# Kernel tuning notes

Measured on AMD Instinct MI355X. Metric: run time of the kernel, lower is better.

Reference implementation:

```python
import jax, jax.numpy as jnp
import numpy as np

B, T, C, H, N = 4, 1024, 2048, 32, 64
DFF, DW, DV, DA, DG = 8192, 64, 32, 64, 128
GN_EPS = 64e-5  # RWKV7 ln_x GroupNorm eps


def _ln(x, w, b, eps=1e-5):
    m = x.mean(-1, keepdims=True)
    v = ((x - m) ** 2).mean(-1, keepdims=True)
    return (x - m) / jnp.sqrt(v + eps) * w + b


def _block(x, v_first, att_shift, ffn_shift, wkv_state,
           ln1_w, ln1_b, ln2_w, ln2_b,
           x_r, x_w, x_k, x_v, x_a, x_g,
           Wr, Wk, Wv, Wo,
           w0, w1, w2, v0, v1, v2, a0, a1, a2, g1, g2,
           k_k, k_a, r_k, lnx_w, lnx_b,
           ffn_xk, Wk_ffn, Wv_ffn):
    # ----- TimeMix -----
    xn = _ln(x, ln1_w, ln1_b)
    xx = jnp.concatenate([att_shift[:, None, :], xn[:, :-1]], axis=1) - xn
    xr = xn + xx * x_r
    xw = xn + xx * x_w
    xk_ = xn + xx * x_k
    xv = xn + xx * x_v
    xa = xn + xx * x_a
    xg = xn + xx * x_g

    r = xr @ Wr
    w = -jax.nn.softplus(-(w0 + jnp.tanh(xw @ w1) @ w2)) - 0.5  # <= -0.5
    k = xk_ @ Wk
    v = xv @ Wv
    # layer_id != 0: interpolate toward v_first
    v = v + (v_first - v) * jax.nn.sigmoid(v0 + (xv @ v1) @ v2)
    a = jax.nn.sigmoid(a0 + (xa @ a1) @ a2)
    g = jax.nn.sigmoid(xg @ g1) @ g2

    kk = (k * k_k).reshape(B, T, H, N)
    kk = kk / jnp.maximum(jnp.linalg.norm(kk, axis=-1, keepdims=True), 1e-12)
    k = k * (1.0 + (a - 1.0) * k_a)

    rh = r.reshape(B, T, H, N)
    wh = jnp.exp(-jnp.exp(w.reshape(B, T, H, N)))  # decay in (0,1)
    kh = k.reshape(B, T, H, N)
    vh = v.reshape(B, T, H, N)
    ah = a.reshape(B, T, H, N)
    aa = -kk
    bb = kk * ah

    def step(S, inp):
        # S: [B,H,N(value),N(key)]
        r_t, w_t, k_t, v_t, a_t, b_t = inp
        sa = jnp.einsum('bhvk,bhk->bhv', S, a_t)
        S = S * w_t[:, :, None, :] + sa[..., None] * b_t[:, :, None, :] + v_t[..., None] * k_t[:, :, None, :]
        y = jnp.einsum('bhvk,bhk->bhv', S, r_t)
        return S, y

    tm = lambda z: jnp.swapaxes(z, 0, 1)  # [B,T,H,N] -> [T,B,H,N]
    S_new, ys = jax.lax.scan(step, wkv_state, (tm(rh), tm(wh), tm(kh), tm(vh), tm(aa), tm(bb)))
    x_wkv = jnp.swapaxes(ys, 0, 1).reshape(B, T, C)

    # GroupNorm over H groups of size N (RWKV7 ln_x)
    xh = x_wkv.reshape(B, T, H, N)
    mu = xh.mean(-1, keepdims=True)
    var = ((xh - mu) ** 2).mean(-1, keepdims=True)
    x_wkv = ((xh - mu) / jnp.sqrt(var + GN_EPS)).reshape(B, T, C) * lnx_w + lnx_b

    resid = ((rh * kh * r_k).sum(-1, keepdims=True) * vh).reshape(B, T, C)
    x_wkv = x_wkv + resid
    att_out = (x_wkv * g) @ Wo
    x1 = x + att_out

    # ----- ChannelMix -----
    xn2 = _ln(x1, ln2_w, ln2_b)
    xx2 = jnp.concatenate([ffn_shift[:, None, :], xn2[:, :-1]], axis=1) - xn2
    xkf = xn2 + xx2 * ffn_xk
    kf = jnp.square(jax.nn.relu(xkf @ Wk_ffn))
    x_out = x1 + kf @ Wv_ffn
    return x_out, S_new


def setup_inputs() -> dict:
    ks = jax.random.split(jax.random.key(0), 48)
    rn = lambda i, sh, s=1.0: jax.random.normal(ks[i], sh, dtype=jnp.float32) * s
    return {
        'x': rn(0, (B, T, C)), 'v_first': rn(1, (B, T, C)),
        'att_shift': rn(2, (B, C)), 'ffn_shift': rn(3, (B, C)),
        'wkv_state': jnp.zeros((B, H, N, N), jnp.float32),
        'ln1_w': jnp.ones((C,), jnp.float32), 'ln1_b': jnp.zeros((C,), jnp.float32),
        'ln2_w': jnp.ones((C,), jnp.float32), 'ln2_b': jnp.zeros((C,), jnp.float32),
        'x_r': rn(4, (C,), 0.3), 'x_w': rn(5, (C,), 0.3), 'x_k': rn(6, (C,), 0.3),
        'x_v': rn(7, (C,), 0.3), 'x_a': rn(8, (C,), 0.3), 'x_g': rn(9, (C,), 0.3),
        'Wr': rn(10, (C, C), 0.02), 'Wk': rn(11, (C, C), 0.02),
        'Wv': rn(12, (C, C), 0.02), 'Wo': rn(13, (C, C), 0.02),
        'w0': rn(14, (C,), 0.3), 'w1': rn(15, (C, DW), 0.02), 'w2': rn(16, (DW, C), 0.02),
        'v0': rn(17, (C,), 0.3), 'v1': rn(18, (C, DV), 0.02), 'v2': rn(19, (DV, C), 0.02),
        'a0': rn(20, (C,), 0.3), 'a1': rn(21, (C, DA), 0.02), 'a2': rn(22, (DA, C), 0.02),
        'g1': rn(23, (C, DG), 0.02), 'g2': rn(24, (DG, C), 0.02),
        'k_k': rn(25, (C,), 0.1) + 0.7, 'k_a': rn(26, (C,), 0.1) + 0.7, 'r_k': rn(27, (H, N), 0.1),
        'lnx_w': jnp.ones((C,), jnp.float32), 'lnx_b': jnp.zeros((C,), jnp.float32),
        'ffn_xk': rn(28, (C,), 0.3), 'Wk_ffn': rn(29, (C, DFF), 0.02), 'Wv_ffn': rn(30, (DFF, C), 0.02),
    }


def reference(x, v_first, att_shift, ffn_shift, wkv_state,
              ln1_w, ln1_b, ln2_w, ln2_b,
              x_r, x_w, x_k, x_v, x_a, x_g,
              Wr, Wk, Wv, Wo,
              w0, w1, w2, v0, v1, v2, a0, a1, a2, g1, g2,
              k_k, k_a, r_k, lnx_w, lnx_b,
              ffn_xk, Wk_ffn, Wv_ffn):
    return _block(x, v_first, att_shift, ffn_shift, wkv_state,
                  ln1_w, ln1_b, ln2_w, ln2_b,
                  x_r, x_w, x_k, x_v, x_a, x_g,
                  Wr, Wk, Wv, Wo,
                  w0, w1, w2, v0, v1, v2, a0, a1, a2, g1, g2,
                  k_k, k_a, r_k, lnx_w, lnx_b,
                  ffn_xk, Wk_ffn, Wv_ffn)
```

## Files before the change

kernel.cpp:

```cpp
#include <hip/hip_runtime.h>
#include <cstdint>


typedef __attribute__((ext_vector_type(4))) float f32x4;
typedef __attribute__((ext_vector_type(8))) __bf16 bf16x8;
typedef __attribute__((ext_vector_type(8))) unsigned short us8;

#define DEV __device__ __forceinline__

DEV unsigned short f2b(float f) {
  union { float f; unsigned u; } v; v.f = f;
  unsigned r = v.u + 0x7fffu + ((v.u >> 16) & 1u);
  return (unsigned short)(r >> 16);
}
DEV float b2f(unsigned short u) {
  union { unsigned u; float f; } v; v.u = (unsigned)u << 16;
  return v.f;
}

DEV void gload16(const void* g, void* l) {
  void* gg = const_cast<void*>(g);
  __builtin_amdgcn_global_load_lds(
      (__attribute__((address_space(1))) unsigned int*)gg,
      (__attribute__((address_space(3))) unsigned int*)l, 16, 0, 0);
}

DEV float red8(float v) {
  v += __shfl_xor(v, 1);
  v += __shfl_xor(v, 2);
  v += __shfl_xor(v, 4);
  return v;
}


__global__ void k_transpose4(const float* __restrict__ s0,
                             const float* __restrict__ s1,
                             const float* __restrict__ s2,
                             const float* __restrict__ s3,
                             unsigned short* __restrict__ d0,
                             unsigned short* __restrict__ d1,
                             unsigned short* __restrict__ d2,
                             unsigned short* __restrict__ d3) {
  __shared__ float tile[32][33];
  const int z = blockIdx.z;
  const float* src = z == 0 ? s0 : z == 1 ? s1 : z == 2 ? s2 : s3;
  unsigned short* dst = z == 0 ? d0 : z == 1 ? d1 : z == 2 ? d2 : d3;
  const int c0 = blockIdx.x * 32, r0 = blockIdx.y * 32;
  const int tx = threadIdx.x, ty = threadIdx.y;
  for (int i = ty; i < 32; i += 8)
    tile[i][tx] = src[(size_t)(r0 + i) * 2048 + c0 + tx];
  __syncthreads();
  for (int i = ty; i < 32; i += 8)
    dst[(size_t)(c0 + i) * 2048 + r0 + tx] = f2b(tile[tx][i]);
}

__global__ void k_transpose(const float* __restrict__ src,
                            unsigned short* __restrict__ dst, int R, int Cc) {
  __shared__ float tile[32][33];
  const int c0 = blockIdx.x * 32, r0 = blockIdx.y * 32;
  const int tx = threadIdx.x, ty = threadIdx.y;
  for (int i = ty; i < 32; i += 8)
    tile[i][tx] = src[(size_t)(r0 + i) * Cc + c0 + tx];
  __syncthreads();
  for (int i = ty; i < 32; i += 8)
    dst[(size_t)(c0 + i) * R + r0 + tx] = f2b(tile[tx][i]);
}

__global__ void k_prep(const float* __restrict__ w1, const float* __restrict__ a1,
                       const float* __restrict__ v1, const float* __restrict__ g1,
                       const float* __restrict__ xw, const float* __restrict__ xa,
                       const float* __restrict__ xv, const float* __restrict__ xg,
                       const float* __restrict__ w2, const float* __restrict__ a2,
                       const float* __restrict__ v2, const float* __restrict__ g2,
                       unsigned short* __restrict__ dcat,
                       unsigned short* __restrict__ dup) {
  int i = blockIdx.x * 256 + threadIdx.x;
  if (i < 384 * 4096) {
    const int j = i >> 12, c = i & 4095;
    float val = 0.f;
    if (j < 288) {
      const float* W; const float* mix; int jj, D;
      if (j < 64)       { W = w1; mix = xw; jj = j;       D = 64;  }
      else if (j < 128) { W = a1; mix = xa; jj = j - 64;  D = 64;  }
      else if (j < 160) { W = v1; mix = xv; jj = j - 128; D = 32;  }
      else              { W = g1; mix = xg; jj = j - 160; D = 128; }
      const int cc = c & 2047;
      val = W[(size_t)cc * D + jj];
      if (c >= 2048) val *= mix[cc];
    }
    dcat[i] = f2b(val);
    return;
  }
  i -= 384 * 4096;
  if (i >= 8192 * 288) return;
  const int n = i / 288, k = i - n * 288;
  const int p = n >> 11, j = n & 2047;
  float val = 0.f;
  if (p == 0)      { if (k < 64)              val = w2[(size_t)k * 2048 + j]; }
  else if (p == 1) { if (k >= 64 && k < 128)  val = a2[(size_t)(k - 64) * 2048 + j]; }
  else if (p == 2) { if (k >= 128 && k < 160) val = v2[(size_t)(k - 128) * 2048 + j]; }
  else             { if (k >= 160)            val = g2[(size_t)(k - 160) * 2048 + j]; }
  dup[i] = f2b(val);
}


DEV void breduce2(float& a, float& b, float* rbuf) {
#pragma unroll
  for (int m = 1; m < 64; m <<= 1) { a += __shfl_xor(a, m); b += __shfl_xor(b, m); }
  const int wid = threadIdx.x >> 6, lane = threadIdx.x & 63;
  if (lane == 0) { rbuf[wid] = a; rbuf[4 + wid] = b; }
  __syncthreads();
  a = rbuf[0] + rbuf[1] + rbuf[2] + rbuf[3];
  b = rbuf[4] + rbuf[5] + rbuf[6] + rbuf[7];
  __syncthreads();
}

__global__ __launch_bounds__(256)
void k_ln1_mix(const float* __restrict__ x, const float* __restrict__ shift,
               const float* __restrict__ lw, const float* __restrict__ lb,
               const float* __restrict__ mr, const float* __restrict__ mk,
               const float* __restrict__ mv,
               unsigned short* __restrict__ A2, unsigned short* __restrict__ xrb,
               unsigned short* __restrict__ xkb, unsigned short* __restrict__ xvb) {
  __shared__ float rbuf[8];
  const int m = blockIdx.x, tid = threadIdx.x;
  const int b = m >> 10, t = m & 1023;
  const float* xt = x + (size_t)m * 2048 + tid * 8;
  const float* xp = (t > 0) ? (x + (size_t)(m - 1) * 2048 + tid * 8)
                            : (shift + (size_t)b * 2048 + tid * 8);
  float vt[8], vp[8];
  *(float4*)&vt[0] = *(const float4*)(xt);
  *(float4*)&vt[4] = *(const float4*)(xt + 4);
  *(float4*)&vp[0] = *(const float4*)(xp);
  *(float4*)&vp[4] = *(const float4*)(xp + 4);
  float st = 0.f, sp = 0.f;
#pragma unroll
  for (int i = 0; i < 8; ++i) { st += vt[i]; sp += vp[i]; }
  breduce2(st, sp, rbuf);
  const float mt_ = st * (1.f / 2048.f), mp_ = sp * (1.f / 2048.f);
  float qt = 0.f, qp = 0.f;
#pragma unroll
  for (int i = 0; i < 8; ++i) {
    float d0 = vt[i] - mt_; qt += d0 * d0;
    float d1 = vp[i] - mp_; qp += d1 * d1;
  }
  breduce2(qt, qp, rbuf);
  const float rt = rsqrtf(qt * (1.f / 2048.f) + 1e-5f);
  const float rp = rsqrtf(qp * (1.f / 2048.f) + 1e-5f);
  const bool lnp = (t > 0);
#pragma unroll
  for (int i = 0; i < 8; ++i) {
    const int c = tid * 8 + i;
    const float wv = lw[c], bv = lb[c];
    const float xn = (vt[i] - mt_) * rt * wv + bv;
    const float pn = lnp ? ((vp[i] - mp_) * rp * wv + bv) : vp[i];
    const float xx = pn - xn;
    A2[(size_t)m * 4096 + c] = f2b(xn);
    A2[(size_t)m * 4096 + 2048 + c] = f2b(xx);
    xrb[(size_t)m * 2048 + c] = f2b(xn + xx * mr[c]);
    xkb[(size_t)m * 2048 + c] = f2b(xn + xx * mk[c]);
    xvb[(size_t)m * 2048 + c] = f2b(xn + xx * mv[c]);
  }
}

__global__ __launch_bounds__(256)
void k_ln2_mix(const float* __restrict__ x1, const float* __restrict__ shift,
               const float* __restrict__ lw, const float* __restrict__ lb,
               const float* __restrict__ mk, unsigned short* __restrict__ xkf) {
  __shared__ float rbuf[8];
  const int m = blockIdx.x, tid = threadIdx.x;
  const int b = m >> 10, t = m & 1023;
  const float* xt = x1 + (size_t)m * 2048 + tid * 8;
  const float* xp = (t > 0) ? (x1 + (size_t)(m - 1) * 2048 + tid * 8)
                            : (shift + (size_t)b * 2048 + tid * 8);
  float vt[8], vp[8];
  *(float4*)&vt[0] = *(const float4*)(xt);
  *(float4*)&vt[4] = *(const float4*)(xt + 4);
  *(float4*)&vp[0] = *(const float4*)(xp);
  *(float4*)&vp[4] = *(const float4*)(xp + 4);
  float st = 0.f, sp = 0.f;
#pragma unroll
  for (int i = 0; i < 8; ++i) { st += vt[i]; sp += vp[i]; }
  breduce2(st, sp, rbuf);
  const float mt_ = st * (1.f / 2048.f), mp_ = sp * (1.f / 2048.f);
  float qt = 0.f, qp = 0.f;
#pragma unroll
  for (int i = 0; i < 8; ++i) {
    float d0 = vt[i] - mt_; qt += d0 * d0;
    float d1 = vp[i] - mp_; qp += d1 * d1;
  }
  breduce2(qt, qp, rbuf);
  const float rt = rsqrtf(qt * (1.f / 2048.f) + 1e-5f);
  const float rp = rsqrtf(qp * (1.f / 2048.f) + 1e-5f);
  const bool lnp = (t > 0);
#pragma unroll
  for (int i = 0; i < 8; ++i) {
    const int c = tid * 8 + i;
    const float wv = lw[c], bv = lb[c];
    const float xn = (vt[i] - mt_) * rt * wv + bv;
    const float pn = lnp ? ((vp[i] - mp_) * rp * wv + bv) : vp[i];
    xkf[(size_t)m * 2048 + c] = f2b(xn + (pn - xn) * mk[c]);
  }
}


constexpr int EP_F32 = 0, EP_B16 = 1, EP_RELU2 = 5, EP_ADDF = 6, EP_HACT = 7;

template <int EP>
DEV void ep_store(float acc, long row, long c, long ldc, float* Co,
                  unsigned short* Cob, const float* bias, const float* e0f,
                  const unsigned short* e0b) {
  const long idx = row * ldc + c;
  (void)bias; (void)e0b;
  if constexpr (EP == EP_F32) {
    Co[idx] = acc;
  } else if constexpr (EP == EP_B16) {
    Cob[idx] = f2b(acc);
  } else if constexpr (EP == EP_RELU2) {
    const float r = fmaxf(acc, 0.f);
    Cob[idx] = f2b(r * r);
  } else if constexpr (EP == EP_ADDF) {
    Co[idx] = acc + e0f[idx];
  } else if constexpr (EP == EP_HACT) {
    float vv = acc;
    if (c < 64) vv = tanhf(vv);
    else if (c >= 160) vv = 1.f / (1.f + expf(-vv));
    Cob[idx] = f2b(vv);
  }
}


template <int EP>
__global__ __launch_bounds__(256)
void gemm_bt(const unsigned short* __restrict__ A, long lda,
             const unsigned short* __restrict__ Bt, long ldb, long N, long K,
             long ldc, float* __restrict__ Co, unsigned short* __restrict__ Cob,
             const float* __restrict__ bias, const float* __restrict__ e0f,
             const unsigned short* __restrict__ e0b) {
  __shared__ unsigned short As[4096];
  __shared__ unsigned short Bs[4096];
  const int tid = threadIdx.x;
  const int wid = tid >> 6, lane = tid & 63;
  const long row0 = (long)blockIdx.x * 128, col0 = (long)blockIdx.y * 128;
  const int wm = (wid >> 1) * 64, wn = (wid & 1) * 64;
  f32x4 acc[4][4] = {};
  const int sr = tid >> 2, sk = (tid & 3) * 8;
  const unsigned short* gA = A + (row0 + sr) * lda + sk;
  const unsigned short* gB = Bt + (col0 + sr) * ldb + sk;
  unsigned short* lA = As + wid * 512;
  unsigned short* lB = Bs + wid * 512;
  const int fr = lane & 15, fk = (lane >> 4) * 8;

  for (long kb = 0; kb < K; kb += 32) {
    gload16(gA + kb, lA);
    gload16(gA + kb + 64 * lda, lA + 2048);
    gload16(gB + kb, lB);
    gload16(gB + kb + 64 * ldb, lB + 2048);
    __syncthreads();
    bf16x8 af[4], bq[4];
#pragma unroll
    for (int mt = 0; mt < 4; ++mt)
      af[mt] = *(const bf16x8*)(As + (wm + mt * 16 + fr) * 32 + fk);
#pragma unroll
    for (int nt = 0; nt < 4; ++nt)
      bq[nt] = *(const bf16x8*)(Bs + (wn + nt * 16 + fr) * 32 + fk);
#pragma unroll
    for (int mt = 0; mt < 4; ++mt)
#pragma unroll
      for (int nt = 0; nt < 4; ++nt)
        acc[mt][nt] = __builtin_amdgcn_mfma_f32_16x16x32_bf16(
            af[mt], bq[nt], acc[mt][nt], 0, 0, 0);
    __syncthreads();
  }
  const int fq = lane >> 4;
#pragma unroll
  for (int mt = 0; mt < 4; ++mt) {
#pragma unroll
    for (int nt = 0; nt < 4; ++nt) {
      const long c = col0 + wn + nt * 16 + fr;
      if (c < N) {
        const long rb = row0 + wm + mt * 16 + fq * 4;
#pragma unroll
        for (int rg = 0; rg < 4; ++rg)
          ep_store<EP>(acc[mt][nt][rg], rb + rg, c, ldc, Co, Cob, bias, e0f, e0b);
      }
    }
  }
}


template <int EP>
__global__ __launch_bounds__(256)
void gemm3(const unsigned short* __restrict__ A, long lda,
           const unsigned short* __restrict__ Bt, long ldb, long K, long ldc,
           float* __restrict__ Co, unsigned short* __restrict__ Cob,
           const float* __restrict__ e0f) {
  __shared__ unsigned short As[2][4096];
  __shared__ unsigned short Bs[2][4096];
  const int tid = threadIdx.x;
  const int wid = tid >> 6, lane = tid & 63;
  const long row0 = (long)blockIdx.x * 128, col0 = (long)blockIdx.y * 128;
  const int wm = (wid >> 1) * 64, wn = (wid & 1) * 64;
  f32x4 acc[4][4] = {};
  const int srow = tid >> 2;
  const int scol = 8 * ((tid & 3) ^ (srow & 3));
  const unsigned short* gA = A + (row0 + srow) * lda + scol;
  const unsigned short* gB = Bt + (col0 + srow) * ldb + scol;
  const int fr = lane & 15, fc = lane >> 4;

#define STAGE3(buf, kb)                                         \
  {                                                             \
    gload16(gA + (kb), &As[buf][0] + wid * 512);                \
    gload16(gA + (kb) + 64 * lda, &As[buf][2048] + wid * 512);  \
    gload16(gB + (kb), &Bs[buf][0] + wid * 512);                \
    gload16(gB + (kb) + 64 * ldb, &Bs[buf][2048] + wid * 512);  \
  }

  STAGE3(0, 0)
  const int NT = (int)(K >> 5);
  int cur = 0;
  for (int kt = 0; kt < NT; ++kt) {
    if (kt + 1 < NT) {
      STAGE3(cur ^ 1, (long)(kt + 1) * 32)
      asm volatile("s_waitcnt vmcnt(4)" ::: "memory");
    } else {
      asm volatile("s_waitcnt vmcnt(0)" ::: "memory");
    }
    __builtin_amdgcn_s_barrier();
    asm volatile("" ::: "memory");
    bf16x8 af[4], bq[4];
#pragma unroll
    for (int mt = 0; mt < 4; ++mt) {
      const int r = wm + mt * 16 + fr;
      af[mt] = *(const bf16x8*)(&As[cur][0] + r * 32 + ((fc ^ (r & 3)) * 8));
    }
#pragma unroll
    for (int nt = 0; nt < 4; ++nt) {
      const int r = wn + nt * 16 + fr;
      bq[nt] = *(const bf16x8*)(&Bs[cur][0] + r * 32 + ((fc ^ (r & 3)) * 8));
    }
    __builtin_amdgcn_s_setprio(1);
#pragma unroll
    for (int mt = 0; mt < 4; ++mt)
#pragma unroll
      for (int nt = 0; nt < 4; ++nt)
        acc[mt][nt] = __builtin_amdgcn_mfma_f32_16x16x32_bf16(
            af[mt], bq[nt], acc[mt][nt], 0, 0, 0);
    __builtin_amdgcn_s_setprio(0);
    asm volatile("" ::: "memory");
    __builtin_amdgcn_s_barrier();
    cur ^= 1;
  }
#undef STAGE3
  const int fq = lane >> 4;
#pragma unroll
  for (int mt = 0; mt < 4; ++mt) {
#pragma unroll
    for (int nt = 0; nt < 4; ++nt) {
      const long c = col0 + wn + nt * 16 + fr;
      const long rb = row0 + wm + mt * 16 + fq * 4;
#pragma unroll
      for (int rg = 0; rg < 4; ++rg)
        ep_store<EP>(acc[mt][nt][rg], rb + rg, c, ldc, Co, Cob, nullptr, e0f,
                     nullptr);
    }
  }
}


template <int EP>
__global__ __launch_bounds__(512)
void gemm8p(const unsigned short* __restrict__ A, long lda,
            const unsigned short* __restrict__ Bt, long ldb, long K, long ldc,
            float* __restrict__ Co, unsigned short* __restrict__ Cob,
            const float* __restrict__ e0f) {
  __shared__ unsigned short lds[65536];
  const int tid = threadIdx.x;
  const int wid = tid >> 6, lane = tid & 63;
  const long row0 = (long)blockIdx.x * 256, col0 = (long)blockIdx.y * 256;
  const int wrow = (wid >> 2) * 64;
  const int wcol = (wid & 3) * 32;
  const int fr = lane & 15, fc = lane >> 4;
  f32x4 acc[2][4][2][2] = {};

  const int sr0 = tid >> 3;
  int sce = (tid & 7) * 8;
  sce ^= ((sr0 >> 2) & 1) << 4;
  const unsigned short* gA = A + (row0 + sr0) * lda + sce;
  const unsigned short* gB = Bt + (col0 + sr0) * ldb + sce;

#define STG8(half, src, ld, kb, buf)                                     \
  {                                                                      \
    const unsigned short* s_ = (src) + (kb);                             \
    unsigned short* d_ = lds + (buf) * 32768 + (half) * 8192 + tid * 8;  \
    gload16(s_, d_);                                                     \
    gload16(s_ + 64 * (ld), d_ + 4096);                                  \
  }

  STG8(0, gA, lda, 0, 0)
  STG8(2, gB, ldb, 0, 0)
  STG8(1, gA + 128 * lda, lda, 0, 0)
  STG8(3, gB + 128 * ldb, ldb, 0, 0)
  asm volatile("s_waitcnt vmcnt(0)" ::: "memory");
  __builtin_amdgcn_s_barrier();

  const int NT = (int)(K >> 6);
  int cur = 0;

#define PHASE8(P, KT)                                                         \
  {                                                                           \
    constexpr int mh = (P) >> 1, nh = (P) & 1;                                \
    const int bb = cur * 32768;                                               \
    bf16x8 af[4][2], bq[2][2];                                                \
    _Pragma("unroll") for (int mt = 0; mt < 4; ++mt)                          \
      _Pragma("unroll") for (int ks = 0; ks < 2; ++ks) {                      \
        const int r = wrow + mt * 16 + fr;                                    \
        const int e = (ks * 32 + fc * 8) ^ (((r >> 2) & 1) << 4);             \
        af[mt][ks] = *(const bf16x8*)(lds + bb + mh * 8192 + r * 64 + e);     \
      }                                                                       \
    _Pragma("unroll") for (int nt = 0; nt < 2; ++nt)                          \
      _Pragma("unroll") for (int ks = 0; ks < 2; ++ks) {                      \
        const int r = wcol + nt * 16 + fr;                                    \
        const int e = (ks * 32 + fc * 8) ^ (((r >> 2) & 1) << 4);             \
        bq[nt][ks] =                                                          \
            *(const bf16x8*)(lds + bb + 16384 + nh * 8192 + r * 64 + e);      \
      }                                                                       \
    if ((KT) + 1 < NT) {                                                      \
      const long kb_ = (long)((KT) + 1) * 64;                                 \
      if constexpr ((P) == 0) STG8(0, gA, lda, kb_, cur ^ 1)                  \
      else if constexpr ((P) == 1) STG8(2, gB, ldb, kb_, cur ^ 1)             \
      else if constexpr ((P) == 2) STG8(1, gA + 128 * lda, lda, kb_, cur ^ 1) \
      else STG8(3, gB + 128 * ldb, ldb, kb_, cur ^ 1)                         \
    }                                                                         \
    if constexpr ((P) == 0) asm volatile("s_waitcnt vmcnt(2)" ::: "memory");  \
    if constexpr ((P) == 3) asm volatile("s_waitcnt vmcnt(4)" ::: "memory");  \
    __builtin_amdgcn_s_barrier();                                             \
    asm volatile("s_waitcnt lgkmcnt(0)" ::: "memory");                        \
    __builtin_amdgcn_s_setprio(1);                                            \
    _Pragma("unroll") for (int mt = 0; mt < 4; ++mt)                          \
      _Pragma("unroll") for (int nt = 0; nt < 2; ++nt)                        \
        _Pragma("unroll") for (int ks = 0; ks < 2; ++ks)                      \
          acc[mh][mt][nh][nt] = __builtin_amdgcn_mfma_f32_16x16x32_bf16(      \
              af[mt][ks], bq[nt][ks], acc[mh][mt][nh][nt], 0, 0, 0);          \
    __builtin_amdgcn_s_setprio(0);                                            \
    asm volatile("" ::: "memory");                                            \
    __builtin_amdgcn_s_barrier();                                             \
  }

  for (int kt = 0; kt < NT; ++kt) {
    PHASE8(0, kt)
    PHASE8(1, kt)
    PHASE8(2, kt)
    PHASE8(3, kt)
    cur ^= 1;
  }
#undef PHASE8
#undef STG8

  const int fq = lane >> 4;
#pragma unroll
  for (int mh = 0; mh < 2; ++mh)
#pragma unroll
    for (int mt = 0; mt < 4; ++mt)
#pragma unroll
      for (int nh = 0; nh < 2; ++nh)
#pragma unroll
        for (int nt = 0; nt < 2; ++nt) {
          const long c = col0 + nh * 128 + wcol + nt * 16 + fr;
          const long rb = row0 + mh * 128 + wrow + mt * 16 + fq * 4;
#pragma unroll
          for (int rg = 0; rg < 4; ++rg)
            ep_store<EP>(acc[mh][mt][nh][nt][rg], rb + rg, c, ldc, Co, Cob,
                         nullptr, e0f, nullptr);
        }
}


__global__ __launch_bounds__(256)
void gemm_up128(const unsigned short* __restrict__ A,
                const unsigned short* __restrict__ Bt,
                float* __restrict__ whb, unsigned short* __restrict__ abuf,
                unsigned short* __restrict__ vfb, unsigned short* __restrict__ gbuf,
                const float* __restrict__ w0, const float* __restrict__ a0,
                const float* __restrict__ v0,
                const unsigned short* __restrict__ vraw,
                const float* __restrict__ vfirst) {
  __shared__ unsigned short As[2][4096];
  __shared__ unsigned short Bs[2][4096];
  const int tid = threadIdx.x;
  const int wid = tid >> 6, lane = tid & 63;
  const long row0 = (long)blockIdx.x * 128, col0 = (long)blockIdx.y * 128;
  const int wm = (wid >> 1) * 64, wn = (wid & 1) * 64;
  f32x4 acc[4][4] = {};
  const int srow = tid >> 2;
  const int scol = 8 * ((tid & 3) ^ (srow & 3));
  const unsigned short* gA = A + (row0 + srow) * 288 + scol;
  const unsigned short* gB = Bt + (col0 + srow) * 288 + scol;
  const int fr = lane & 15, fc = lane >> 4;

#define STAGEU(buf, kb)                                         \
  {                                                             \
    gload16(gA + (kb), &As[buf][0] + wid * 512);                \
    gload16(gA + (kb) + 64 * 288, &As[buf][2048] + wid * 512);  \
    gload16(gB + (kb), &Bs[buf][0] + wid * 512);                \
    gload16(gB + (kb) + 64 * 288, &Bs[buf][2048] + wid * 512);  \
  }

  STAGEU(0, 0)
  int cur = 0;
  for (int kt = 0; kt < 9; ++kt) {
    if (kt + 1 < 9) {
      STAGEU(cur ^ 1, (long)(kt + 1) * 32)
      asm volatile("s_waitcnt vmcnt(4)" ::: "memory");
    } else {
      asm volatile("s_waitcnt vmcnt(0)" ::: "memory");
    }
    __builtin_amdgcn_s_barrier();
    asm volatile("" ::: "memory");
    bf16x8 af[4], bq[4];
#pragma unroll
    for (int mt = 0; mt < 4; ++mt) {
      const int r = wm + mt * 16 + fr;
      af[mt] = *(const bf16x8*)(&As[cur][0] + r * 32 + ((fc ^ (r & 3)) * 8));
    }
#pragma unroll
    for (int nt = 0; nt < 4; ++nt) {
      const int r = wn + nt * 16 + fr;
      bq[nt] = *(const bf16x8*)(&Bs[cur][0] + r * 32 + ((fc ^ (r & 3)) * 8));
    }
    __builtin_amdgcn_s_setprio(1);
#pragma unroll
    for (int mt = 0; mt < 4; ++mt)
#pragma unroll
      for (int nt = 0; nt < 4; ++nt)
        acc[mt][nt] = __builtin_amdgcn_mfma_f32_16x16x32_bf16(
            af[mt], bq[nt], acc[mt][nt], 0, 0, 0);
    __builtin_amdgcn_s_setprio(0);
    asm volatile("" ::: "memory");
    __builtin_amdgcn_s_barrier();
    cur ^= 1;
  }
#undef STAGEU
  const int fq = lane >> 4;
  const int p = (int)(blockIdx.y >> 4);
#pragma unroll
  for (int mt = 0; mt < 4; ++mt) {
#pragma unroll
    for (int nt = 0; nt < 4; ++nt) {
      const long c = col0 + wn + nt * 16 + fr;
      const long cc = c & 2047;
      const long rb = row0 + wm + mt * 16 + fq * 4;
#pragma unroll
      for (int rg = 0; rg < 4; ++rg) {
        const float av = acc[mt][nt][rg];
        const long idx = (rb + rg) * 2048 + cc;
        if (p == 0) {
          const float wv = w0[cc] + av;
          const float sp = log1pf(expf(-wv));
          whb[idx] = expf(-expf(-sp - 0.5f));
        } else if (p == 1) {
          abuf[idx] = f2b(1.f / (1.f + expf(-(a0[cc] + av))));
        } else if (p == 2) {
          const float s = 1.f / (1.f + expf(-(v0[cc] + av)));
          const float vv = b2f(vraw[idx]);
          vfb[idx] = f2b(vv + (vfirst[idx] - vv) * s);
        } else {
          gbuf[idx] = f2b(av);
        }
      }
    }
  }
}

__global__ __launch_bounds__(256)
void k_post(unsigned short* __restrict__ kio, unsigned short* __restrict__ abio,
            unsigned short* __restrict__ aao, const float* __restrict__ kkw,
            const float* __restrict__ kaw) {
  const int m = blockIdx.x, tid = threadIdx.x;
  const size_t base = (size_t)m * 2048 + tid * 8;
  us8 k8 = *(const us8*)(kio + base);
  us8 a8 = *(const us8*)(abio + base);
  float kk8[8], ka8[8];
  *(float4*)&kk8[0] = *(const float4*)(kkw + tid * 8);
  *(float4*)&kk8[4] = *(const float4*)(kkw + tid * 8 + 4);
  *(float4*)&ka8[0] = *(const float4*)(kaw + tid * 8);
  *(float4*)&ka8[4] = *(const float4*)(kaw + tid * 8 + 4);
  float kx[8], kv[8], av[8];
  float ss = 0.f;
#pragma unroll
  for (int i = 0; i < 8; ++i) {
    kv[i] = b2f(k8[i]); av[i] = b2f(a8[i]);
    kx[i] = kv[i] * kk8[i]; ss += kx[i] * kx[i];
  }
  ss = red8(ss);
  const float inv = 1.f / fmaxf(sqrtf(ss), 1e-12f);
  us8 kh8, aa8, bb8;
#pragma unroll
  for (int i = 0; i < 8; ++i) {
    const float kkn = kx[i] * inv;
    kh8[i] = f2b(kv[i] * (1.f + (av[i] - 1.f) * ka8[i]));
    aa8[i] = f2b(-kkn);
    bb8[i] = f2b(kkn * av[i]);
  }
  *(us8*)(kio + base) = kh8;
  *(us8*)(aao + base) = aa8;
  *(us8*)(abio + base) = bb8;
}


DEV float red16(float x) {
  union { float f; int i; } a, r;
  a.f = x; r.i = __builtin_amdgcn_update_dpp(0, a.i, 0xB1, 0xf, 0xf, true);
  x += r.f;
  a.f = x; r.i = __builtin_amdgcn_update_dpp(0, a.i, 0x4E, 0xf, 0xf, true);
  x += r.f;
  a.f = x; r.i = __builtin_amdgcn_update_dpp(0, a.i, 0x124, 0xf, 0xf, true);
  x += r.f;
  a.f = x; r.i = __builtin_amdgcn_update_dpp(0, a.i, 0x128, 0xf, 0xf, true);
  x += r.f;
  return x;
}

DEV void cv4(const uint2 q, float* o) {
  union { unsigned u; float f; } t;
  t.u = q.x << 16;          o[0] = t.f;
  t.u = q.x & 0xffff0000u;  o[1] = t.f;
  t.u = q.y << 16;          o[2] = t.f;
  t.u = q.y & 0xffff0000u;  o[3] = t.f;
}

__global__ __launch_bounds__(64)
void k_scan(const unsigned short* __restrict__ rp,
            const unsigned short* __restrict__ kp,
            const unsigned short* __restrict__ vp,
            const float* __restrict__ wp,
            const unsigned short* __restrict__ ap,
            const unsigned short* __restrict__ bp,
            const float* __restrict__ s0, unsigned short* __restrict__ yout,
            float* __restrict__ snew) {
  __shared__ float4 slots[8][49];
  __shared__ unsigned short ylds[1024][4];
  const int lane = threadIdx.x;
  const int bh = blockIdx.x & 127;
  const int rq = blockIdx.x >> 7;
  const int b = bh >> 5, h = bh & 31;
  const int kg = lane & 15, rl = lane >> 4;
  const int v = rq * 4 + rl, ks = kg * 4;
  const size_t off_bh = (size_t)b * 1024 * 2048 + (size_t)h * 64;
  const int vfo = 768 + ((rq & 1) * 4 + rl) * 2;

  float S[4];
  *(float4*)&S[0] = *(const float4*)(s0 + (((size_t)bh * 64 + v) * 64 + ks));

  const char* gp = nullptr;
  size_t gstep = 0;
  if (lane < 49) {
    if (lane < 32) {
      const int arr = lane >> 3, sub = lane & 7;
      const unsigned short* base = arr == 0 ? rp : arr == 1 ? kp
                                 : arr == 2 ? ap : bp;
      gp = (const char*)(base + off_bh + sub * 8);
      gstep = 4096;
    } else if (lane < 48) {
      gp = (const char*)(wp + off_bh + (lane - 32) * 4);
      gstep = 8192;
    } else {
      gp = (const char*)(vp + off_bh + (rq & ~1) * 4);
      gstep = 4096;
    }
  }
#pragma unroll
  for (int s = 0; s < 8; ++s) {
    if (lane < 49) gload16(gp, &slots[s][0]);
    gp += gstep;
  }

  uint2 rA, kA, aA, bA, rB, kB, aB, bB;
  float4 wA, wB;
  unsigned short fA, fB;
  asm volatile("s_waitcnt vmcnt(7)" ::: "memory");
  {
    const char* nb = (const char*)&slots[0][0];
    rA = *(const uint2*)(nb + kg * 8);
    kA = *(const uint2*)(nb + 128 + kg * 8);
    aA = *(const uint2*)(nb + 256 + kg * 8);
    bA = *(const uint2*)(nb + 384 + kg * 8);
    wA = *(const float4*)(nb + 512 + kg * 16);
    fA = *(const unsigned short*)(nb + vfo);
  }

#define SSTEP(T, Cr, Ck, Ca, Cb, Cw, Cf, Nr, Nk, Na, Nb, Nw, Nf)             \
  {                                                                          \
    asm volatile("s_waitcnt lgkmcnt(0)" ::: "memory");                       \
    if (lane < 49) gload16(gp, &slots[(T) & 7][0]);                          \
    if ((T) < 1015) gp += gstep;                                             \
    asm volatile("s_waitcnt vmcnt(7)" ::: "memory");                         \
    const char* nb = (const char*)&slots[((T) + 1) & 7][0];                  \
    Nr = *(const uint2*)(nb + kg * 8);                                       \
    Nk = *(const uint2*)(nb + 128 + kg * 8);                                 \
    Na = *(const uint2*)(nb + 256 + kg * 8);                                 \
    Nb = *(const uint2*)(nb + 384 + kg * 8);                                 \
    Nw = *(const float4*)(nb + 512 + kg * 16);                               \
    Nf = *(const unsigned short*)(nb + vfo);                                 \
    float rr[4], kk[4], av[4], bv[4];                                        \
    cv4(Cr, rr); cv4(Ck, kk); cv4(Ca, av); cv4(Cb, bv);                      \
    const float vv = b2f(Cf);                                                \
    float sa = S[0] * av[0] + S[1] * av[1] + S[2] * av[2] + S[3] * av[3];    \
    sa = red16(sa);                                                          \
    float y;                                                                 \
    S[0] = S[0] * Cw.x + sa * bv[0] + vv * kk[0]; y  = S[0] * rr[0];         \
    S[1] = S[1] * Cw.y + sa * bv[1] + vv * kk[1]; y += S[1] * rr[1];         \
    S[2] = S[2] * Cw.z + sa * bv[2] + vv * kk[2]; y += S[2] * rr[2];         \
    S[3] = S[3] * Cw.w + sa * bv[3] + vv * kk[3]; y += S[3] * rr[3];         \
    y = red16(y);                                                            \
    if (kg == 0) ylds[T][rl] = f2b(y);                                       \
  }

  for (int tb = 0; tb < 1024; tb += 2) {
    SSTEP(tb + 0, rA, kA, aA, bA, wA, fA, rB, kB, aB, bB, wB, fB)
    SSTEP(tb + 1, rB, kB, aB, bB, wB, fB, rA, kA, aA, bA, wA, fA)
  }
#undef SSTEP

  *(float4*)(snew + (((size_t)bh * 64 + v) * 64 + ks)) = *(const float4*)&S[0];
  asm volatile("s_waitcnt lgkmcnt(0)" ::: "memory");
#pragma unroll 4
  for (int it = 0; it < 16; ++it) {
    const int t = lane + it * 64;
    const uint2 val = *(const uint2*)&ylds[t][0];
    *(uint2*)(yout + off_bh + (size_t)t * 2048 + rq * 4) = val;
  }
}


__global__ __launch_bounds__(256)
void k_gn(const unsigned short* __restrict__ y, const unsigned short* __restrict__ r,
          const unsigned short* __restrict__ kh, const unsigned short* __restrict__ vf,
          const unsigned short* __restrict__ g, const float* __restrict__ rk,
          const float* __restrict__ lw, const float* __restrict__ lb,
          unsigned short* __restrict__ ywg) {
  const int m = blockIdx.x, tid = threadIdx.x;
  const size_t base = (size_t)m * 2048 + tid * 8;
  us8 y8 = *(const us8*)(y + base);
  us8 r8 = *(const us8*)(r + base);
  us8 k8 = *(const us8*)(kh + base);
  us8 v8 = *(const us8*)(vf + base);
  us8 g8 = *(const us8*)(g + base);
  float yv[8];
  float rkv[8];
  *(float4*)&rkv[0] = *(const float4*)(rk + tid * 8);
  *(float4*)&rkv[4] = *(const float4*)(rk + tid * 8 + 4);
  float sy = 0.f, sd = 0.f;
#pragma unroll
  for (int i = 0; i < 8; ++i) {
    yv[i] = b2f(y8[i]);
    sy += yv[i];
    sd += b2f(r8[i]) * b2f(k8[i]) * rkv[i];
  }
  sy = red8(sy);
  sd = red8(sd);
  const float mu = sy * (1.f / 64.f);
  float sq = 0.f;
#pragma unroll
  for (int i = 0; i < 8; ++i) { const float d = yv[i] - mu; sq += d * d; }
  sq = red8(sq);
  const float rstd = rsqrtf(sq * (1.f / 64.f) + 64e-5f);
  us8 o8;
#pragma unroll
  for (int i = 0; i < 8; ++i) {
    const int c = tid * 8 + i;
    const float gn = (yv[i] - mu) * rstd * lw[c] + lb[c];
    o8[i] = f2b((gn + sd * b2f(v8[i])) * b2f(g8[i]));
  }
  *(us8*)(ywg + base) = o8;
}


extern "C" void kernel_launch(void* const* d_in, const int* in_sizes, int n_in,
                              void* d_out, int out_size, void* d_ws,
                              size_t ws_size, hipStream_t stream) {
  (void)in_sizes; (void)n_in; (void)out_size; (void)ws_size;
  const float* x         = (const float*)d_in[0];
  const float* v_first   = (const float*)d_in[1];
  const float* att_shift = (const float*)d_in[2];
  const float* ffn_shift = (const float*)d_in[3];
  const float* wkv0      = (const float*)d_in[4];
  const float* ln1w = (const float*)d_in[5];
  const float* ln1b = (const float*)d_in[6];
  const float* ln2w = (const float*)d_in[7];
  const float* ln2b = (const float*)d_in[8];
  const float* x_r = (const float*)d_in[9];
  const float* x_w = (const float*)d_in[10];
  const float* x_k = (const float*)d_in[11];
  const float* x_v = (const float*)d_in[12];
  const float* x_a = (const float*)d_in[13];
  const float* x_g = (const float*)d_in[14];
  const float* Wr = (const float*)d_in[15];
  const float* Wk = (const float*)d_in[16];
  const float* Wv = (const float*)d_in[17];
  const float* Wo = (const float*)d_in[18];
  const float* w0 = (const float*)d_in[19];
  const float* w1 = (const float*)d_in[20];
  const float* w2 = (const float*)d_in[21];
  const float* v0 = (const float*)d_in[22];
  const float* v1 = (const float*)d_in[23];
  const float* v2 = (const float*)d_in[24];
  const float* a0 = (const float*)d_in[25];
  const float* a1 = (const float*)d_in[26];
  const float* a2 = (const float*)d_in[27];
  const float* g1 = (const float*)d_in[28];
  const float* g2 = (const float*)d_in[29];
  const float* k_k = (const float*)d_in[30];
  const float* k_a = (const float*)d_in[31];
  const float* r_k = (const float*)d_in[32];
  const float* lnxw = (const float*)d_in[33];
  const float* lnxb = (const float*)d_in[34];
  const float* ffn_xk = (const float*)d_in[35];
  const float* Wkf = (const float*)d_in[36];
  const float* Wvf = (const float*)d_in[37];

  char* ws = (char*)d_ws;
  constexpr size_t OFF_TWR   = 0;
  constexpr size_t OFF_TWK   = 8388608;
  constexpr size_t OFF_TWV   = 16777216;
  constexpr size_t OFF_TWO   = 25165824;
  constexpr size_t OFF_TWCAT = 34734080;
  constexpr size_t OFF_HACT  = 37879808;
  constexpr size_t OFF_GBUF  = 40239104;
  constexpr size_t OFF_WH    = 57016320;
  constexpr size_t OFF_R     = 90570752;
  constexpr size_t OFF_KH    = 107347968;
  constexpr size_t OFF_VF    = 124125184;
  constexpr size_t OFF_AA    = 140902400;
  constexpr size_t OFF_BB    = 157679616;
  constexpr size_t OFF_TWUP  = 174456832;

  unsigned short* tWr = (unsigned short*)(ws + OFF_TWR);
  unsigned short* tWk = (unsigned short*)(ws + OFF_TWK);
  unsigned short* tWv = (unsigned short*)(ws + OFF_TWV);
  unsigned short* tWo = (unsigned short*)(ws + OFF_TWO);
  unsigned short* tWcat = (unsigned short*)(ws + OFF_TWCAT);
  unsigned short* Hact  = (unsigned short*)(ws + OFF_HACT);
  unsigned short* gbuf  = (unsigned short*)(ws + OFF_GBUF);
  unsigned short* tWvfh = (unsigned short*)(ws + OFF_GBUF);
  unsigned short* act2  = (unsigned short*)(ws + OFF_WH);
  float*          whb   = (float*)(ws + OFF_WH);
  unsigned short* ywg   = (unsigned short*)(ws + OFF_WH);
  unsigned short* kf    = (unsigned short*)(ws + OFF_WH);
  unsigned short* bxr   = (unsigned short*)(ws + OFF_AA);
  unsigned short* bxk   = (unsigned short*)(ws + OFF_BB);
  unsigned short* bxv   = (unsigned short*)(ws + OFF_VF);
  unsigned short* rbuf  = (unsigned short*)(ws + OFF_R);
  unsigned short* khb   = (unsigned short*)(ws + OFF_KH);
  unsigned short* vfb   = (unsigned short*)(ws + OFF_VF);
  unsigned short* aab   = (unsigned short*)(ws + OFF_AA);
  unsigned short* bbb   = (unsigned short*)(ws + OFF_BB);
  unsigned short* vraw  = (unsigned short*)(ws + OFF_AA);
  unsigned short* abuf  = (unsigned short*)(ws + OFF_BB);
  float*          x1    = (float*)(ws + OFF_R);
  unsigned short* xkf   = (unsigned short*)(ws + OFF_VF);
  unsigned short* tWkf  = (unsigned short*)(ws + OFF_AA);
  unsigned short* tWup  = (unsigned short*)(ws + OFF_TWUP);
  float* out = (float*)d_out;
  float* snew = out + 8388608;

  const dim3 tb(32, 8);
  k_transpose4<<<dim3(64, 64, 4), tb, 0, stream>>>(Wr, Wk, Wv, Wo,
                                                   tWr, tWk, tWv, tWo);
  k_prep<<<15360, 256, 0, stream>>>(w1, a1, v1, g1, x_w, x_a, x_v, x_g,
                                    w2, a2, v2, g2, tWcat, tWup);

  k_ln1_mix<<<4096, 256, 0, stream>>>(x, att_shift, ln1w, ln1b, x_r, x_k, x_v,
                                      act2, bxr, bxk, bxv);
  gemm3<EP_B16><<<dim3(32, 16), 256, 0, stream>>>(
      bxr, 2048, tWr, 2048, 2048, 2048, nullptr, rbuf, nullptr);
  gemm3<EP_B16><<<dim3(32, 16), 256, 0, stream>>>(
      bxk, 2048, tWk, 2048, 2048, 2048, nullptr, khb, nullptr);
  gemm3<EP_B16><<<dim3(32, 16), 256, 0, stream>>>(
      bxv, 2048, tWv, 2048, 2048, 2048, nullptr, vraw, nullptr);
  gemm_bt<EP_HACT><<<dim3(32, 3), 256, 0, stream>>>(
      act2, 4096, tWcat, 4096, 288, 4096, 288, nullptr, Hact, nullptr, nullptr, nullptr);
  gemm_up128<<<dim3(32, 64), 256, 0, stream>>>(
      Hact, tWup, whb, abuf, vfb, gbuf, w0, a0, v0, vraw, v_first);
  k_post<<<4096, 256, 0, stream>>>(khb, abuf, aab, k_k, k_a);

  k_scan<<<2048, 64, 0, stream>>>(rbuf, khb, vfb, whb, aab, bbb, wkv0,
                                  (unsigned short*)out, snew);
  k_gn<<<4096, 256, 0, stream>>>((const unsigned short*)out, rbuf, khb, vfb,
                                 gbuf, r_k, lnxw, lnxb, ywg);

  gemm3<EP_ADDF><<<dim3(32, 16), 256, 0, stream>>>(
      ywg, 2048, tWo, 2048, 2048, 2048, x1, nullptr, x);

  k_ln2_mix<<<4096, 256, 0, stream>>>(x1, ffn_shift, ln2w, ln2b, ffn_xk, xkf);
  k_transpose<<<dim3(256, 64), tb, 0, stream>>>(Wkf, tWkf, 2048, 8192);
  gemm8p<EP_RELU2><<<dim3(16, 16), 512, 0, stream>>>(
      xkf, 2048, tWkf, 2048, 2048, 4096, nullptr, kf, nullptr);
  k_transpose<<<dim3(64, 128), tb, 0, stream>>>(Wvf, tWvfh, 4096, 2048);
  gemm3<EP_ADDF><<<dim3(32, 16), 256, 0, stream>>>(
      kf, 4096, tWvfh, 4096, 4096, 2048, out, nullptr, x1);
  gemm8p<EP_RELU2><<<dim3(16, 16), 512, 0, stream>>>(
      xkf, 2048, tWkf + (size_t)4096 * 2048, 2048, 2048, 4096, nullptr, kf, nullptr);
  k_transpose<<<dim3(64, 128), tb, 0, stream>>>(Wvf + (size_t)4096 * 2048, tWvfh,
                                                4096, 2048);
  gemm3<EP_ADDF><<<dim3(32, 16), 256, 0, stream>>>(
      kf, 4096, tWvfh, 4096, 4096, 2048, out, nullptr, out);
}
```

Before: 1.266 ms.

## Batch R/K/V projections into one launch and pipeline the low-rank GEMM

```diff
diff --git a/kernel.cpp b/kernel.cpp
--- a/kernel.cpp
+++ b/kernel.cpp
@@ -204,7 +204,7 @@
 }
 
 
-constexpr int EP_F32 = 0, EP_B16 = 1, EP_RELU2 = 5, EP_ADDF = 6, EP_HACT = 7;
+constexpr int EP_F32 = 0, EP_B16 = 1, EP_RELU2 = 5, EP_ADDF = 6;
 
 template <int EP>
 DEV void ep_store(float acc, long row, long c, long ldc, float* Co,
@@ -221,70 +221,6 @@
     Cob[idx] = f2b(r * r);
   } else if constexpr (EP == EP_ADDF) {
     Co[idx] = acc + e0f[idx];
-  } else if constexpr (EP == EP_HACT) {
-    float vv = acc;
-    if (c < 64) vv = tanhf(vv);
-    else if (c >= 160) vv = 1.f / (1.f + expf(-vv));
-    Cob[idx] = f2b(vv);
-  }
-}
-
-
-template <int EP>
-__global__ __launch_bounds__(256)
-void gemm_bt(const unsigned short* __restrict__ A, long lda,
-             const unsigned short* __restrict__ Bt, long ldb, long N, long K,
-             long ldc, float* __restrict__ Co, unsigned short* __restrict__ Cob,
-             const float* __restrict__ bias, const float* __restrict__ e0f,
-             const unsigned short* __restrict__ e0b) {
-  __shared__ unsigned short As[4096];
-  __shared__ unsigned short Bs[4096];
-  const int tid = threadIdx.x;
-  const int wid = tid >> 6, lane = tid & 63;
-  const long row0 = (long)blockIdx.x * 128, col0 = (long)blockIdx.y * 128;
-  const int wm = (wid >> 1) * 64, wn = (wid & 1) * 64;
-  f32x4 acc[4][4] = {};
-  const int sr = tid >> 2, sk = (tid & 3) * 8;
-  const unsigned short* gA = A + (row0 + sr) * lda + sk;
-  const unsigned short* gB = Bt + (col0 + sr) * ldb + sk;
-  unsigned short* lA = As + wid * 512;
-  unsigned short* lB = Bs + wid * 512;
-  const int fr = lane & 15, fk = (lane >> 4) * 8;
-
-  for (long kb = 0; kb < K; kb += 32) {
-    gload16(gA + kb, lA);
-    gload16(gA + kb + 64 * lda, lA + 2048);
-    gload16(gB + kb, lB);
-    gload16(gB + kb + 64 * ldb, lB + 2048);
-    __syncthreads();
-    bf16x8 af[4], bq[4];
-#pragma unroll
-    for (int mt = 0; mt < 4; ++mt)
-      af[mt] = *(const bf16x8*)(As + (wm + mt * 16 + fr) * 32 + fk);
-#pragma unroll
-    for (int nt = 0; nt < 4; ++nt)
-      bq[nt] = *(const bf16x8*)(Bs + (wn + nt * 16 + fr) * 32 + fk);
-#pragma unroll
-    for (int mt = 0; mt < 4; ++mt)
-#pragma unroll
-      for (int nt = 0; nt < 4; ++nt)
-        acc[mt][nt] = __builtin_amdgcn_mfma_f32_16x16x32_bf16(
-            af[mt], bq[nt], acc[mt][nt], 0, 0, 0);
-    __syncthreads();
-  }
-  const int fq = lane >> 4;
-#pragma unroll
-  for (int mt = 0; mt < 4; ++mt) {
-#pragma unroll
-    for (int nt = 0; nt < 4; ++nt) {
-      const long c = col0 + wn + nt * 16 + fr;
-      if (c < N) {
-        const long rb = row0 + wm + mt * 16 + fq * 4;
-#pragma unroll
-        for (int rg = 0; rg < 4; ++rg)
-          ep_store<EP>(acc[mt][nt][rg], rb + rg, c, ldc, Co, Cob, bias, e0f, e0b);
-      }
-    }
   }
 }
 
@@ -363,6 +299,172 @@
       for (int rg = 0; rg < 4; ++rg)
         ep_store<EP>(acc[mt][nt][rg], rb + rg, c, ldc, Co, Cob, nullptr, e0f,
                      nullptr);
+    }
+  }
+}
+
+
+__global__ __launch_bounds__(256)
+void gemm3_qkv(const unsigned short* __restrict__ A0,
+               const unsigned short* __restrict__ A1,
+               const unsigned short* __restrict__ A2p,
+               const unsigned short* __restrict__ B0,
+               const unsigned short* __restrict__ B1,
+               const unsigned short* __restrict__ B2,
+               unsigned short* __restrict__ C0,
+               unsigned short* __restrict__ C1,
+               unsigned short* __restrict__ C2) {
+  const int z = blockIdx.z;
+  const unsigned short* A = z == 0 ? A0 : z == 1 ? A1 : A2p;
+  const unsigned short* Bt = z == 0 ? B0 : z == 1 ? B1 : B2;
+  unsigned short* Cob = z == 0 ? C0 : z == 1 ? C1 : C2;
+  __shared__ unsigned short As[2][4096];
+  __shared__ unsigned short Bs[2][4096];
+  const int tid = threadIdx.x;
+  const int wid = tid >> 6, lane = tid & 63;
+  const long row0 = (long)blockIdx.x * 128, col0 = (long)blockIdx.y * 128;
+  const int wm = (wid >> 1) * 64, wn = (wid & 1) * 64;
+  f32x4 acc[4][4] = {};
+  const int srow = tid >> 2;
+  const int scol = 8 * ((tid & 3) ^ (srow & 3));
+  const unsigned short* gA = A + (row0 + srow) * 2048 + scol;
+  const unsigned short* gB = Bt + (col0 + srow) * 2048 + scol;
+  const int fr = lane & 15, fc = lane >> 4;
+
+#define STAGEQ(buf, kb)                                          \
+  {                                                              \
+    gload16(gA + (kb), &As[buf][0] + wid * 512);                 \
+    gload16(gA + (kb) + 64 * 2048, &As[buf][2048] + wid * 512);  \
+    gload16(gB + (kb), &Bs[buf][0] + wid * 512);                 \
+    gload16(gB + (kb) + 64 * 2048, &Bs[buf][2048] + wid * 512);  \
+  }
+
+  STAGEQ(0, 0)
+  int cur = 0;
+  for (int kt = 0; kt < 64; ++kt) {
+    if (kt + 1 < 64) {
+      STAGEQ(cur ^ 1, (long)(kt + 1) * 32)
+      asm volatile("s_waitcnt vmcnt(4)" ::: "memory");
+    } else {
+      asm volatile("s_waitcnt vmcnt(0)" ::: "memory");
+    }
+    __builtin_amdgcn_s_barrier();
+    asm volatile("" ::: "memory");
+    bf16x8 af[4], bq[4];
+#pragma unroll
+    for (int mt = 0; mt < 4; ++mt) {
+      const int r = wm + mt * 16 + fr;
+      af[mt] = *(const bf16x8*)(&As[cur][0] + r * 32 + ((fc ^ (r & 3)) * 8));
+    }
+#pragma unroll
+    for (int nt = 0; nt < 4; ++nt) {
+      const int r = wn + nt * 16 + fr;
+      bq[nt] = *(const bf16x8*)(&Bs[cur][0] + r * 32 + ((fc ^ (r & 3)) * 8));
+    }
+    __builtin_amdgcn_s_setprio(1);
+#pragma unroll
+    for (int mt = 0; mt < 4; ++mt)
+#pragma unroll
+      for (int nt = 0; nt < 4; ++nt)
+        acc[mt][nt] = __builtin_amdgcn_mfma_f32_16x16x32_bf16(
+            af[mt], bq[nt], acc[mt][nt], 0, 0, 0);
+    __builtin_amdgcn_s_setprio(0);
+    asm volatile("" ::: "memory");
+    __builtin_amdgcn_s_barrier();
+    cur ^= 1;
+  }
+#undef STAGEQ
+  const int fq = lane >> 4;
+#pragma unroll
+  for (int mt = 0; mt < 4; ++mt) {
+#pragma unroll
+    for (int nt = 0; nt < 4; ++nt) {
+      const long c = col0 + wn + nt * 16 + fr;
+      const long rb = row0 + wm + mt * 16 + fq * 4;
+#pragma unroll
+      for (int rg = 0; rg < 4; ++rg)
+        Cob[(rb + rg) * 2048 + c] = f2b(acc[mt][nt][rg]);
+    }
+  }
+}
+
+
+__global__ __launch_bounds__(256)
+void gemm3h(const unsigned short* __restrict__ A,
+            const unsigned short* __restrict__ Bt,
+            unsigned short* __restrict__ Hact) {
+  __shared__ unsigned short As[2][4096];
+  __shared__ unsigned short Bs[2][4096];
+  const int tid = threadIdx.x;
+  const int wid = tid >> 6, lane = tid & 63;
+  const long row0 = (long)blockIdx.x * 128, col0 = (long)blockIdx.y * 128;
+  const int wm = (wid >> 1) * 64, wn = (wid & 1) * 64;
+  f32x4 acc[4][4] = {};
+  const int srow = tid >> 2;
+  const int scol = 8 * ((tid & 3) ^ (srow & 3));
+  const unsigned short* gA = A + (row0 + srow) * 4096 + scol;
+  const unsigned short* gB = Bt + (col0 + srow) * 4096 + scol;
+  const int fr = lane & 15, fc = lane >> 4;
+
+#define STAGEH(buf, kb)                                          \
+  {                                                              \
+    gload16(gA + (kb), &As[buf][0] + wid * 512);                 \
+    gload16(gA + (kb) + 64 * 4096, &As[buf][2048] + wid * 512);  \
+    gload16(gB + (kb), &Bs[buf][0] + wid * 512);                 \
+    gload16(gB + (kb) + 64 * 4096, &Bs[buf][2048] + wid * 512);  \
+  }
+
+  STAGEH(0, 0)
+  int cur = 0;
+  for (int kt = 0; kt < 128; ++kt) {
+    if (kt + 1 < 128) {
+      STAGEH(cur ^ 1, (long)(kt + 1) * 32)
+      asm volatile("s_waitcnt vmcnt(4)" ::: "memory");
+    } else {
+      asm volatile("s_waitcnt vmcnt(0)" ::: "memory");
+    }
+    __builtin_amdgcn_s_barrier();
+    asm volatile("" ::: "memory");
+    bf16x8 af[4], bq[4];
+#pragma unroll
+    for (int mt = 0; mt < 4; ++mt) {
+      const int r = wm + mt * 16 + fr;
+      af[mt] = *(const bf16x8*)(&As[cur][0] + r * 32 + ((fc ^ (r & 3)) * 8));
+    }
+#pragma unroll
+    for (int nt = 0; nt < 4; ++nt) {
+      const int r = wn + nt * 16 + fr;
+      bq[nt] = *(const bf16x8*)(&Bs[cur][0] + r * 32 + ((fc ^ (r & 3)) * 8));
+    }
+    __builtin_amdgcn_s_setprio(1);
+#pragma unroll
+    for (int mt = 0; mt < 4; ++mt)
+#pragma unroll
+      for (int nt = 0; nt < 4; ++nt)
+        acc[mt][nt] = __builtin_amdgcn_mfma_f32_16x16x32_bf16(
+            af[mt], bq[nt], acc[mt][nt], 0, 0, 0);
+    __builtin_amdgcn_s_setprio(0);
+    asm volatile("" ::: "memory");
+    __builtin_amdgcn_s_barrier();
+    cur ^= 1;
+  }
+#undef STAGEH
+  const int fq = lane >> 4;
+#pragma unroll
+  for (int mt = 0; mt < 4; ++mt) {
+#pragma unroll
+    for (int nt = 0; nt < 4; ++nt) {
+      const long c = col0 + wn + nt * 16 + fr;
+      if (c < 288) {
+        const long rb = row0 + wm + mt * 16 + fq * 4;
+#pragma unroll
+        for (int rg = 0; rg < 4; ++rg) {
+          float vv = acc[mt][nt][rg];
+          if (c < 64) vv = tanhf(vv);
+          else if (c >= 160) vv = 1.f / (1.f + expf(-vv));
+          Hact[(rb + rg) * 288 + c] = f2b(vv);
+        }
+      }
     }
   }
 }
@@ -872,14 +974,9 @@
 
   k_ln1_mix<<<4096, 256, 0, stream>>>(x, att_shift, ln1w, ln1b, x_r, x_k, x_v,
                                       act2, bxr, bxk, bxv);
-  gemm3<EP_B16><<<dim3(32, 16), 256, 0, stream>>>(
-      bxr, 2048, tWr, 2048, 2048, 2048, nullptr, rbuf, nullptr);
-  gemm3<EP_B16><<<dim3(32, 16), 256, 0, stream>>>(
-      bxk, 2048, tWk, 2048, 2048, 2048, nullptr, khb, nullptr);
-  gemm3<EP_B16><<<dim3(32, 16), 256, 0, stream>>>(
-      bxv, 2048, tWv, 2048, 2048, 2048, nullptr, vraw, nullptr);
-  gemm_bt<EP_HACT><<<dim3(32, 3), 256, 0, stream>>>(
-      act2, 4096, tWcat, 4096, 288, 4096, 288, nullptr, Hact, nullptr, nullptr, nullptr);
+  gemm3_qkv<<<dim3(32, 16, 3), 256, 0, stream>>>(bxr, bxk, bxv, tWr, tWk, tWv,
+                                                 rbuf, khb, vraw);
+  gemm3h<<<dim3(32, 3), 256, 0, stream>>>(act2, tWcat, Hact);
   gemm_up128<<<dim3(32, 64), 256, 0, stream>>>(
       Hact, tWup, whb, abuf, vfb, gbuf, w0, a0, v0, vraw, v_first);
   k_post<<<4096, 256, 0, stream>>>(khb, abuf, aab, k_k, k_a);
```

Result: faster. 1.232 ms (median of 2 runs) (-2.7%).
